# Performance work log

Measured on AMD Instinct MI355X. Metric: run time of the kernel, lower is better.

## Reference

```python
import jax, jax.numpy as jnp
import numpy as np

EPS = 1e-3          # keras BatchNormalization default epsilon
DT = 0.2
LAM2 = 4.0          # lambda_diffusion**2 = 2.0**2
K = 5

def _bn(x, gamma, beta, mean, var):
    # inference-mode batch norm over channel (last) axis
    return (x - mean) * jax.lax.rsqrt(var + EPS) * gamma + beta

def _conv(x, w):
    # NHWC 'same' conv, stride 1, no bias
    return jax.lax.conv_general_dilated(x, w, (1, 1), 'SAME',
                                        dimension_numbers=('NHWC', 'HWIO', 'NHWC'))

def _sobel_edges(x):
    # tf.image.sobel_edges: per-channel 3x3 Sobel with REFLECT padding.
    # returns (dy, dx) matching sobel[...,0], sobel[...,1]
    p = jnp.pad(x, ((0, 0), (1, 1), (1, 1), (0, 0)), mode='reflect')
    dy = (p[:, 2:, :-2] + 2 * p[:, 2:, 1:-1] + p[:, 2:, 2:]) \
       - (p[:, :-2, :-2] + 2 * p[:, :-2, 1:-1] + p[:, :-2, 2:])
    dx = (p[:, :-2, 2:] + 2 * p[:, 1:-1, 2:] + p[:, 2:, 2:]) \
       - (p[:, :-2, :-2] + 2 * p[:, 1:-1, :-2] + p[:, 2:, :-2])
    return dy, dx

def setup_inputs() -> dict:
    key = jax.random.key(0)
    k1, k2, k3 = jax.random.split(key, 3)
    B, H, W, Cin, Cout = 16, 128, 128, 64, 64
    c = jnp.float32
    return {
        'x':   jax.random.normal(k1, (B, H, W, Cin), dtype=c),
        'f_w': jax.random.normal(k2, (3, 3, Cin, Cout), dtype=c) * 0.05,
        'g_w': jax.random.normal(k3, (3, 3, Cout, Cout), dtype=c) * 0.05,
        'bnf_gamma': jnp.ones((Cin,), c),  'bnf_beta': jnp.zeros((Cin,), c),
        'bnf_mean':  jnp.zeros((Cin,), c), 'bnf_var':  jnp.ones((Cin,), c),
        'bng_gamma': jnp.ones((Cout,), c), 'bng_beta': jnp.zeros((Cout,), c),
        'bng_mean':  jnp.zeros((Cout,), c),'bng_var':  jnp.ones((Cout,), c),
        'bno_gamma': jnp.ones((Cout,), c), 'bno_beta': jnp.zeros((Cout,), c),
        'bno_mean':  jnp.zeros((Cout,), c),'bno_var':  jnp.ones((Cout,), c),
    }

def reference(x, f_w, g_w,
              bnf_gamma, bnf_beta, bnf_mean, bnf_var,
              bng_gamma, bng_beta, bng_mean, bng_var,
              bno_gamma, bno_beta, bno_mean, bno_var):
    f = _conv(jax.nn.relu(_bn(x, bnf_gamma, bnf_beta, bnf_mean, bnf_var)), f_w)
    h = f
    g = _conv(jax.nn.relu(_bn(h, bng_gamma, bng_beta, bng_mean, bng_var)), g_w)
    g1 = g
    dy, dx = _sobel_edges(h)
    Dx = 1.0 / (dy * dy / LAM2 + 1.0)   # source: sobel[..., 0]
    Dy = 1.0 / (dx * dx / LAM2 + 1.0)   # source: sobel[..., 1]
    # NOTE: faithful to source — rolls on axis=2 (W) and axis=3 (channels in NHWC)
    ux = 0.5 * (jnp.roll(g, 1, axis=2) - jnp.roll(g, -1, axis=2))
    vy = 0.5 * (jnp.roll(g1, 1, axis=3) - jnp.roll(g1, -1, axis=3))
    Ax = g * DT
    Ay = g1 * DT
    Bx = Dx * DT
    By = Dy * DT
    E = (ux + vy) * DT
    D = 1.0 / (1.0 + 2 * Bx + 2 * By)
    h0 = h
    for _ in range(K):
        prev = h
        h = D * ((1 - 2 * Bx - 2 * By) * h0
                 - 2 * E * h
                 + (-Ax + 2 * Bx) * jnp.roll(h, 1, axis=2)
                 + ( Ax + 2 * Bx) * jnp.roll(h, -1, axis=2)
                 + (-Ay + 2 * By) * jnp.roll(h, 1, axis=3)
                 + ( Ay + 2 * By) * jnp.roll(h, -1, axis=3)
                 + 2 * DT * f)
        h0 = prev
    h = jax.nn.relu(_bn(h, bno_gamma, bno_beta, bno_mean, bno_var))
    return (h, g)
```

## Files before the change

kernel.cpp:

```cpp
#include <hip/hip_runtime.h>

#define HH 128
#define WW 128
#define CC 64
#define ROW (WW*CC)
#define PADW 72

typedef _Float16 half8 __attribute__((ext_vector_type(8)));
typedef _Float16 half4v __attribute__((ext_vector_type(4)));
typedef float floatx4 __attribute__((ext_vector_type(4)));

__global__ __launch_bounds__(256)
void repack_w(const float* __restrict__ wf, const float* __restrict__ wg,
              _Float16* __restrict__ W2f, _Float16* __restrict__ W2g)
{
    int idx = blockIdx.x * 256 + threadIdx.x;
    int sel = idx >= 36864;
    int id  = sel ? idx - 36864 : idx;
    const float* src = sel ? wg : wf;
    _Float16* dst = sel ? W2g : W2f;
    int t = id >> 12, c = (id >> 6) & 63, o = id & 63;
    int kc = c >> 5, q = (c >> 3) & 3, j = c & 7;
    int pos = ((((t*2 + kc)*4 + q)*64 + o) << 3) + j;
    dst[pos] = (_Float16)src[id];
}

template<int BNIN, int EPI>
__global__ __launch_bounds__(256, 2)
void conv_mfma(const void* __restrict__ srcv, const _Float16* __restrict__ W2,
               _Float16* __restrict__ outH, float* __restrict__ outF,
               _Float16* __restrict__ y2,
               const float* __restrict__ ig, const float* __restrict__ ib,
               const float* __restrict__ imu, const float* __restrict__ iva,
               const float* __restrict__ og, const float* __restrict__ ob,
               const float* __restrict__ om, const float* __restrict__ ov)
{
    __shared__ _Float16 sIn[4*130*PADW];
    const int t = threadIdx.x;
    const int blk = blockIdx.x;
    const int b = blk >> 6, i0 = (blk & 63) * 2;

    const int c8 = (t & 7) << 3;
    float scv[8], biv[8];
    if (BNIN) {
        #pragma unroll
        for (int j = 0; j < 8; ++j) {
            float s = ig[c8+j] * rsqrtf(iva[c8+j] + 1e-3f);
            scv[j] = s; biv[j] = ib[c8+j] - imu[c8+j]*s;
        }
    }

    for (int r = 0; r < 4; ++r) {
        int iy = i0 - 1 + r;
        bool inb = (iy >= 0) && (iy < HH);
        #pragma unroll
        for (int k = 0; k < 4; ++k) {
            int idx = t + (k << 8);
            int px = idx >> 3;
            half8 v = {0,0,0,0,0,0,0,0};
            if (inb) {
                if (BNIN) {
                    const float* gp = (const float*)srcv
                        + ((size_t)(b*HH + iy))*ROW + px*CC + c8;
                    float4 u0 = *(const float4*)gp;
                    float4 u1 = *(const float4*)(gp + 4);
                    v[0] = (_Float16)fmaxf(0.f, u0.x*scv[0] + biv[0]);
                    v[1] = (_Float16)fmaxf(0.f, u0.y*scv[1] + biv[1]);
                    v[2] = (_Float16)fmaxf(0.f, u0.z*scv[2] + biv[2]);
                    v[3] = (_Float16)fmaxf(0.f, u0.w*scv[3] + biv[3]);
                    v[4] = (_Float16)fmaxf(0.f, u1.x*scv[4] + biv[4]);
                    v[5] = (_Float16)fmaxf(0.f, u1.y*scv[5] + biv[5]);
                    v[6] = (_Float16)fmaxf(0.f, u1.z*scv[6] + biv[6]);
                    v[7] = (_Float16)fmaxf(0.f, u1.w*scv[7] + biv[7]);
                } else {
                    v = *(const half8*)((const _Float16*)srcv
                        + ((size_t)(b*HH + iy))*ROW + px*CC + c8);
                }
            }
            *(half8*)(sIn + (r*130 + px + 1)*PADW + c8) = v;
        }
    }
    if (t < 128) {
        int rr = t >> 5, s = (t >> 4) & 1, c4 = (t & 15) << 2;
        int slot = s ? 129 : 0;
        half4v z = {0,0,0,0};
        *(half4v*)(sIn + (rr*130 + slot)*PADW + c4) = z;
    }
    __syncthreads();

    const int wv = t >> 6, lane = t & 63;
    const int lm = lane & 15, quad = lane >> 4;
    const int r  = wv >> 1;
    const int px0 = (wv & 1) * 64;
    floatx4 z4 = {0.f,0.f,0.f,0.f};
    floatx4 acc[4][4];
    #pragma unroll
    for (int ms = 0; ms < 4; ++ms)
        #pragma unroll
        for (int nt = 0; nt < 4; ++nt) acc[ms][nt] = z4;

    #pragma unroll
    for (int tap = 0; tap < 9; ++tap) {
        const int di = tap / 3, dj = tap % 3;
        #pragma unroll
        for (int kc = 0; kc < 2; ++kc) {
            const _Float16* ab = sIn + ((r + di)*130 + px0 + lm + dj)*PADW
                               + kc*32 + quad*8;
            half8 a0 = *(const half8*)(ab);
            half8 a1 = *(const half8*)(ab + 16*PADW);
            half8 a2 = *(const half8*)(ab + 32*PADW);
            half8 a3 = *(const half8*)(ab + 48*PADW);
            const _Float16* wb = W2 + (((tap*2 + kc)*4 + quad) << 9) + (lm << 3);
            half8 b0 = *(const half8*)(wb);
            half8 b1 = *(const half8*)(wb + 128);
            half8 b2 = *(const half8*)(wb + 256);
            half8 b3 = *(const half8*)(wb + 384);
            acc[0][0] = __builtin_amdgcn_mfma_f32_16x16x32_f16(a0, b0, acc[0][0], 0,0,0);
            acc[1][0] = __builtin_amdgcn_mfma_f32_16x16x32_f16(a1, b0, acc[1][0], 0,0,0);
            acc[2][0] = __builtin_amdgcn_mfma_f32_16x16x32_f16(a2, b0, acc[2][0], 0,0,0);
            acc[3][0] = __builtin_amdgcn_mfma_f32_16x16x32_f16(a3, b0, acc[3][0], 0,0,0);
            acc[0][1] = __builtin_amdgcn_mfma_f32_16x16x32_f16(a0, b1, acc[0][1], 0,0,0);
            acc[1][1] = __builtin_amdgcn_mfma_f32_16x16x32_f16(a1, b1, acc[1][1], 0,0,0);
            acc[2][1] = __builtin_amdgcn_mfma_f32_16x16x32_f16(a2, b1, acc[2][1], 0,0,0);
            acc[3][1] = __builtin_amdgcn_mfma_f32_16x16x32_f16(a3, b1, acc[3][1], 0,0,0);
            acc[0][2] = __builtin_amdgcn_mfma_f32_16x16x32_f16(a0, b2, acc[0][2], 0,0,0);
            acc[1][2] = __builtin_amdgcn_mfma_f32_16x16x32_f16(a1, b2, acc[1][2], 0,0,0);
            acc[2][2] = __builtin_amdgcn_mfma_f32_16x16x32_f16(a2, b2, acc[2][2], 0,0,0);
            acc[3][2] = __builtin_amdgcn_mfma_f32_16x16x32_f16(a3, b2, acc[3][2], 0,0,0);
            acc[0][3] = __builtin_amdgcn_mfma_f32_16x16x32_f16(a0, b3, acc[0][3], 0,0,0);
            acc[1][3] = __builtin_amdgcn_mfma_f32_16x16x32_f16(a1, b3, acc[1][3], 0,0,0);
            acc[2][3] = __builtin_amdgcn_mfma_f32_16x16x32_f16(a2, b3, acc[2][3], 0,0,0);
            acc[3][3] = __builtin_amdgcn_mfma_f32_16x16x32_f16(a3, b3, acc[3][3], 0,0,0);
        }
    }

    const size_t obase = ((size_t)(b*HH + i0 + r)) * ROW;
    #pragma unroll
    for (int nt = 0; nt < 4; ++nt) {
        int c = nt*16 + lm;
        float s = 0.f, bi2 = 0.f;
        if (EPI) {
            s = og[c] * rsqrtf(ov[c] + 1e-3f);
            bi2 = ob[c] - om[c]*s;
        }
        #pragma unroll
        for (int ms = 0; ms < 4; ++ms) {
            int pix = px0 + ms*16 + quad*4;
            floatx4 v = acc[ms][nt];
            #pragma unroll
            for (int rv = 0; rv < 4; ++rv) {
                size_t o = obase + (size_t)(pix + rv)*CC + c;
                if (EPI) {
                    outH[o] = (_Float16)v[rv];
                    y2[o]   = (_Float16)fmaxf(0.f, v[rv]*s + bi2);
                } else {
                    outF[o] = v[rv];
                }
            }
        }
    }
}

__global__ __launch_bounds__(1024, 2)
void diffuse(const _Float16* __restrict__ f, const float* __restrict__ g,
             float* __restrict__ out,
             const float* __restrict__ bog, const float* __restrict__ bob,
             const float* __restrict__ bom, const float* __restrict__ bov)
{
    __shared__ float B0[ROW], B1[ROW];
    const int t = threadIdx.x;
    const int rowb = blockIdx.x;
    const int b = rowb >> 7, i = rowb & 127;
    const int im = (i == 0)    ? 1    : i - 1;
    const int ip = (i == HH-1) ? HH-2 : i + 1;
    const _Float16* fb  = f + (size_t)b * (HH*ROW);
    const _Float16* frm = fb + (size_t)im * ROW;
    const _Float16* fr0 = fb + (size_t)i  * ROW;
    const _Float16* frp = fb + (size_t)ip * ROW;
    const float* grow = g + (size_t)rowb * ROW;

    const int lane = t & 63;
    const int srcm = (lane & 48) | ((lane - 1) & 15);
    const int srcp = (lane & 48) | ((lane + 1) & 15);
    const int w0 = t >> 4, c0 = (t & 15) << 2;
    const int qch[2] = { t*4, t*4 + 4096 };
    const int wch[2] = { w0, w0 + 64 };

    #pragma unroll
    for (int k = 0; k < 2; ++k) {
        half4v vm = *(const half4v*)(frm + qch[k]);
        half4v vp = *(const half4v*)(frp + qch[k]);
        floatx4 a = { (float)vm[0], (float)vm[1], (float)vm[2], (float)vm[3] };
        floatx4 p = { (float)vp[0], (float)vp[1], (float)vp[2], (float)vp[3] };
        *(floatx4*)(B0 + qch[k]) = a;
        *(floatx4*)(B1 + qch[k]) = p;
    }
    __syncthreads();

    floatx4 Bx4[2], dxp4[2];
    #pragma unroll
    for (int k = 0; k < 2; ++k) {
        int w = wch[k];
        int wm = (w == 0)    ? 1      : w - 1;
        int wp = (w == WW-1) ? WW - 2 : w + 1;
        floatx4 am = *(const floatx4*)(B0 + wm*CC + c0);
        floatx4 a0 = *(const floatx4*)(B0 + w *CC + c0);
        floatx4 ap = *(const floatx4*)(B0 + wp*CC + c0);
        floatx4 bm = *(const floatx4*)(B1 + wm*CC + c0);
        floatx4 b0 = *(const floatx4*)(B1 + w *CC + c0);
        floatx4 bp = *(const floatx4*)(B1 + wp*CC + c0);
        floatx4 dy = (bm + 2.f*b0 + bp) - (am + 2.f*a0 + ap);
        Bx4[k]  = 0.2f / (dy*dy*0.25f + 1.f);
        dxp4[k] = (ap - am) + (bp - bm);
    }
    __syncthreads();

    #pragma unroll
    for (int k = 0; k < 2; ++k) {
        half4v v0 = *(const half4v*)(fr0 + qch[k]);
        floatx4 fv = { (float)v0[0], (float)v0[1], (float)v0[2], (float)v0[3] };
        *(floatx4*)(B0 + qch[k]) = fv;
        *(floatx4*)(B1 + qch[k]) = *(const floatx4*)(grow + qch[k]);
    }
    __syncthreads();

    floatx4 P4[2], R4[2], Q4[2], cH0[2], cEE[2], cF[2], h4[2], h04[2];
    #pragma unroll
    for (int k = 0; k < 2; ++k) {
        int w = wch[k];
        int wm = (w == 0)    ? 1      : w - 1;
        int wp = (w == WW-1) ? WW - 2 : w + 1;
        int wl = (w + WW - 1) & (WW - 1);
        int wr = (w + 1) & (WW - 1);
        floatx4 fm = *(const floatx4*)(B0 + wm*CC + c0);
        floatx4 fv = *(const floatx4*)(B0 + w *CC + c0);
        floatx4 fp = *(const floatx4*)(B0 + wp*CC + c0);
        floatx4 dx = dxp4[k] + 2.f*(fp - fm);
        floatx4 By = 0.2f / (dx*dx*0.25f + 1.f);
        floatx4 Bx = Bx4[k];
        floatx4 gv = *(const floatx4*)(B1 + w *CC + c0);
        floatx4 gl = *(const floatx4*)(B1 + wl*CC + c0);
        floatx4 gr = *(const floatx4*)(B1 + wr*CC + c0);
        float gdm = __shfl(gv[3], srcm, 64);
        float gup = __shfl(gv[0], srcp, 64);
        floatx4 gd = { gdm, gv[0], gv[1], gv[2] };
        floatx4 gu = { gv[1], gv[2], gv[3], gup };
        floatx4 E  = ((gl - gr) + (gd - gu)) * 0.1f;
        floatx4 A  = gv * 0.2f;
        floatx4 Dd = 1.f / (1.f + 2.f*Bx + 2.f*By);
        cH0[k] = 2.f*Dd - 1.f;
        cEE[k] = -2.f * E * Dd;
        P4[k]  = 2.f * Bx * Dd;
        R4[k]  = 2.f * By * Dd;
        Q4[k]  = A * Dd;
        cF[k]  = 0.4f * Dd * fv;
        h4[k] = fv; h04[k] = fv;
    }
    __syncthreads();

    int oWl[2], oWr[2];
    #pragma unroll
    for (int k = 0; k < 2; ++k) {
        int w = wch[k];
        oWl[k] = ((w + WW - 1) & (WW - 1))*CC + c0;
        oWr[k] = ((w + 1) & (WW - 1))*CC + c0;
    }

    float* cur = B0;
    float* oth = B1;
    for (int it = 0; it < 5; ++it) {
        #pragma unroll
        for (int k = 0; k < 2; ++k) {
            floatx4 hl = *(const floatx4*)(cur + oWl[k]);
            floatx4 hr = *(const floatx4*)(cur + oWr[k]);
            floatx4 hv = h4[k];
            float hdm = __shfl(hv[3], srcm, 64);
            float hup = __shfl(hv[0], srcp, 64);
            floatx4 hd = { hdm, hv[0], hv[1], hv[2] };
            floatx4 hu = { hv[1], hv[2], hv[3], hup };
            floatx4 hn = cH0[k]*h04[k] + cEE[k]*hv
                       + P4[k]*(hl + hr) + R4[k]*(hd + hu)
                       + Q4[k]*((hr - hl) + (hu - hd)) + cF[k];
            *(floatx4*)(oth + qch[k]) = hn;
            h04[k] = hv; h4[k] = hn;
        }
        __syncthreads();
        float* tmp = cur; cur = oth; oth = tmp;
    }

    floatx4 gg = *(const floatx4*)(bog + c0);
    floatx4 vv = *(const floatx4*)(bov + c0);
    floatx4 bb = *(const floatx4*)(bob + c0);
    floatx4 mm = *(const floatx4*)(bom + c0);
    floatx4 s4, bi4;
    #pragma unroll
    for (int j = 0; j < 4; ++j) s4[j] = gg[j] * rsqrtf(vv[j] + 1e-3f);
    bi4 = bb - mm*s4;
    float* op = out + (size_t)rowb * ROW;
    #pragma unroll
    for (int k = 0; k < 2; ++k) {
        floatx4 rr = h4[k]*s4 + bi4;
        #pragma unroll
        for (int j = 0; j < 4; ++j) rr[j] = fmaxf(0.f, rr[j]);
        *(floatx4*)(op + qch[k]) = rr;
    }
}

extern "C" void kernel_launch(void* const* d_in, const int* in_sizes, int n_in,
                              void* d_out, int out_size, void* d_ws, size_t ws_size,
                              hipStream_t stream)
{
    const float* x    = (const float*)d_in[0];
    const float* f_w  = (const float*)d_in[1];
    const float* g_w  = (const float*)d_in[2];
    const float* bnf_g = (const float*)d_in[3];
    const float* bnf_b = (const float*)d_in[4];
    const float* bnf_m = (const float*)d_in[5];
    const float* bnf_v = (const float*)d_in[6];
    const float* bng_g = (const float*)d_in[7];
    const float* bng_b = (const float*)d_in[8];
    const float* bng_m = (const float*)d_in[9];
    const float* bng_v = (const float*)d_in[10];
    const float* bno_g = (const float*)d_in[11];
    const float* bno_b = (const float*)d_in[12];
    const float* bno_m = (const float*)d_in[13];
    const float* bno_v = (const float*)d_in[14];

    float* out = (float*)d_out;
    const size_t N = (size_t)16 * HH * WW * CC;
    _Float16* y2   = (_Float16*)d_ws;
    _Float16* fbuf = y2 + N;
    _Float16* W2f  = y2 + 2*N;
    _Float16* W2g  = W2f + 36864;

    repack_w<<<288, 256, 0, stream>>>(f_w, g_w, W2f, W2g);
    conv_mfma<1,1><<<1024, 256, 0, stream>>>(x, W2f, fbuf, nullptr, y2,
                                             bnf_g, bnf_b, bnf_m, bnf_v,
                                             bng_g, bng_b, bng_m, bng_v);
    conv_mfma<0,0><<<1024, 256, 0, stream>>>(y2, W2g, nullptr, out + N, nullptr,
                                             nullptr, nullptr, nullptr, nullptr,
                                             nullptr, nullptr, nullptr, nullptr);
    diffuse<<<2048, 1024, 0, stream>>>(fbuf, out + N, out, bno_g, bno_b, bno_m, bno_v);
}
```

Before: 379.0 us.

## Stage conv epilogue through LDS for vectorized stores and remap block order

```diff
diff --git a/kernel.cpp b/kernel.cpp
--- a/kernel.cpp
+++ b/kernel.cpp
@@ -35,9 +35,9 @@
                const float* __restrict__ og, const float* __restrict__ ob,
                const float* __restrict__ om, const float* __restrict__ ov)
 {
-    __shared__ _Float16 sIn[4*130*PADW];
+    __shared__ __align__(16) _Float16 sIn[4*130*PADW];
     const int t = threadIdx.x;
-    const int blk = blockIdx.x;
+    const int blk = ((blockIdx.x & 7) << 7) | (blockIdx.x >> 3);
     const int b = blk >> 6, i0 = (blk & 63) * 2;
 
     const int c8 = (t & 7) << 3;
@@ -134,29 +134,52 @@
         }
     }
 
-    const size_t obase = ((size_t)(b*HH + i0 + r)) * ROW;
+    __syncthreads();
+    float* sF = (float*)sIn;
     #pragma unroll
     for (int nt = 0; nt < 4; ++nt) {
         int c = nt*16 + lm;
-        float s = 0.f, bi2 = 0.f;
-        if (EPI) {
-            s = og[c] * rsqrtf(ov[c] + 1e-3f);
-            bi2 = ob[c] - om[c]*s;
-        }
         #pragma unroll
         for (int ms = 0; ms < 4; ++ms) {
-            int pix = px0 + ms*16 + quad*4;
+            int pix = r*128 + px0 + ms*16 + quad*4;
             floatx4 v = acc[ms][nt];
             #pragma unroll
-            for (int rv = 0; rv < 4; ++rv) {
-                size_t o = obase + (size_t)(pix + rv)*CC + c;
-                if (EPI) {
-                    outH[o] = (_Float16)v[rv];
-                    y2[o]   = (_Float16)fmaxf(0.f, v[rv]*s + bi2);
-                } else {
-                    outF[o] = v[rv];
-                }
+            for (int rv = 0; rv < 4; ++rv)
+                sF[(pix + rv)*64 + c] = v[rv];
+        }
+    }
+    __syncthreads();
+
+    const size_t gbase = ((size_t)(b*HH + i0)) * ROW;
+    if (EPI) {
+        const int c8o = (t & 7) << 3;
+        float s8[8], bb8[8];
+        #pragma unroll
+        for (int j = 0; j < 8; ++j) {
+            float ss = og[c8o+j] * rsqrtf(ov[c8o+j] + 1e-3f);
+            s8[j] = ss; bb8[j] = ob[c8o+j] - om[c8o+j]*ss;
+        }
+        #pragma unroll
+        for (int jj = 0; jj < 8; ++jj) {
+            int e = (jj*256 + t) << 3;
+            floatx4 u0 = *(const floatx4*)(sF + e);
+            floatx4 u1 = *(const floatx4*)(sF + e + 4);
+            half8 hv, yv;
+            #pragma unroll
+            for (int j = 0; j < 4; ++j) {
+                hv[j]   = (_Float16)u0[j];
+                hv[4+j] = (_Float16)u1[j];
+                yv[j]   = (_Float16)fmaxf(0.f, u0[j]*s8[j]   + bb8[j]);
+                yv[4+j] = (_Float16)fmaxf(0.f, u1[j]*s8[4+j] + bb8[4+j]);
             }
+            *(half8*)(outH + gbase + e) = hv;
+            *(half8*)(y2   + gbase + e) = yv;
+        }
+    } else {
+        #pragma unroll
+        for (int jj = 0; jj < 16; ++jj) {
+            int e = (jj*256 + t) << 2;
+            *(floatx4*)(outF + gbase + e) = *(const floatx4*)(sF + e);
         }
     }
 }
@@ -169,7 +192,7 @@
 {
     __shared__ float B0[ROW], B1[ROW];
     const int t = threadIdx.x;
-    const int rowb = blockIdx.x;
+    const int rowb = ((blockIdx.x & 7) << 8) | (blockIdx.x >> 3);
     const int b = rowb >> 7, i = rowb & 127;
     const int im = (i == 0)    ? 1    : i - 1;
     const int ip = (i == HH-1) ? HH-2 : i + 1;
```

After: 344.1 us. 1.1x faster.
